# Kernel tuning notes

Measured on AMD Instinct MI355X. Metric: run time of the kernel, lower is better.

## Reference

```python
import jax, jax.numpy as jnp
import numpy as np

DIM = 1024
N_HEADS = 16
HEAD_DIM = DIM // N_HEADS


def setup_inputs() -> dict:
    key = jax.random.key(0)
    ks = jax.random.split(key, 5)
    B, L = 2, 2048
    q = jax.random.normal(ks[0], (B, L, DIM), dtype=jnp.float32)
    # nn.Linear weights: shape [out_features, in_features], applied as x @ W.T
    scale = 1.0 / np.sqrt(DIM)
    Wq = jax.random.normal(ks[1], (DIM, DIM), dtype=jnp.float32) * scale
    Wk = jax.random.normal(ks[2], (DIM, DIM), dtype=jnp.float32) * scale
    Wv = jax.random.normal(ks[3], (DIM, DIM), dtype=jnp.float32) * scale
    Wo = jax.random.normal(ks[4], (DIM, DIM), dtype=jnp.float32) * scale
    return {"q": q, "Wq": Wq, "Wk": Wk, "Wv": Wv, "Wo": Wo}


def reference(q, Wq, Wk, Wv, Wo):
    B, L, _ = q.shape
    kv = q  # self-attention (kv=None path)
    # projections: x @ W.T, then split heads: b l (h d) -> b h l d
    def split_heads(x):
        return x.reshape(B, L, N_HEADS, HEAD_DIM).transpose(0, 2, 1, 3)
    qh = split_heads(q @ Wq.T)
    kh = split_heads(kv @ Wk.T)
    vh = split_heads(kv @ Wv.T)
    # scaled dot-product attention; scale = sqrt(head_dim)
    scores = jnp.einsum('bhid,bhjd->bhij', qh, kh) / jnp.sqrt(
        jnp.asarray(HEAD_DIM, dtype=qh.dtype))
    attn = jax.nn.softmax(scores, axis=-1)
    out = jnp.einsum('bhij,bhjd->bhid', attn, vh)
    # b h l d -> b l (h d)
    out = out.transpose(0, 2, 1, 3).reshape(B, L, DIM)
    return out @ Wo.T
```

## Files before the change

### kernel.cpp

```cpp
#include <hip/hip_runtime.h>


#define DIMN 1024
#define NH 16
#define HD 64
#define BB 2
#define LL 2048

typedef float f32x4 __attribute__((ext_vector_type(4)));
typedef short s16x8 __attribute__((ext_vector_type(8)));

#define QSCALE 0.18033688011112042f

static __device__ __forceinline__ unsigned short f2bf(float f) {
  unsigned u = __float_as_uint(f);
  u += 0x7fffu + ((u >> 16) & 1u);
  return (unsigned short)(u >> 16);
}
static __device__ __forceinline__ unsigned packbf2(float lo, float hi) {
  return (unsigned)f2bf(lo) | ((unsigned)f2bf(hi) << 16);
}
static __device__ __forceinline__ float xexp2(float x) {
#if __has_builtin(__builtin_amdgcn_exp2f)
  return __builtin_amdgcn_exp2f(x);
#else
  return exp2f(x);
#endif
}
static __device__ __forceinline__ s16x8 cvt8(float4 a, float4 b) {
  s16x8 r;
  r[0] = (short)f2bf(a.x); r[1] = (short)f2bf(a.y);
  r[2] = (short)f2bf(a.z); r[3] = (short)f2bf(a.w);
  r[4] = (short)f2bf(b.x); r[5] = (short)f2bf(b.y);
  r[6] = (short)f2bf(b.z); r[7] = (short)f2bf(b.w);
  return r;
}
static __device__ __forceinline__ void gld16(const unsigned short* g,
                                             unsigned short* l) {
#if __has_builtin(__builtin_amdgcn_global_load_lds)
  __builtin_amdgcn_global_load_lds(
      (const __attribute__((address_space(1))) void*)g,
      (__attribute__((address_space(3))) void*)l, 16, 0, 0);
#else
  ((uint4*)l)[threadIdx.x & 63] = ((const uint4*)g)[0];
#endif
}

static __device__ __forceinline__ int vpos(int s128) {
  return (s128 & 0x60) | ((s128 & 0x0C) << 1) | ((s128 & 0x10) >> 2) | (s128 & 3);
}

__global__ __launch_bounds__(256) void cvt_all(
    const float* __restrict__ X, const float* __restrict__ Wq,
    const float* __restrict__ Wk, const float* __restrict__ Wv,
    const float* __restrict__ Wo, unsigned short* __restrict__ out) {
  const int blk = blockIdx.x;
  const float* src;
  unsigned short* dst;
  size_t off;
  if (blk < 2048) {
    src = X; dst = out; off = (size_t)blk * 2048;
  } else {
    int s = (blk - 2048) >> 9;
    src = (s == 0) ? Wq : (s == 1) ? Wk : (s == 2) ? Wv : Wo;
    dst = out + ((size_t)1 << 22) + (size_t)s * (1u << 20);
    off = (size_t)((blk - 2048) & 511) * 2048;
  }
  size_t i = off + (size_t)threadIdx.x * 8;
  float4 v0 = *(const float4*)(src + i);
  float4 v1 = *(const float4*)(src + i + 4);
  uint4 o;
  o.x = packbf2(v0.x, v0.y); o.y = packbf2(v0.z, v0.w);
  o.z = packbf2(v1.x, v1.y); o.w = packbf2(v1.z, v1.w);
  *(uint4*)(dst + i) = o;
}

__global__ __launch_bounds__(256) void gemm_qkv(
    const unsigned short* __restrict__ Xb, const unsigned short* __restrict__ Wb,
    unsigned short* __restrict__ Qb, unsigned short* __restrict__ Kb,
    unsigned short* __restrict__ VT) {
  __shared__ __align__(16) unsigned short Al[128 * 64];
  __shared__ __align__(16) unsigned short Bl[128 * 64];
  const int lin = blockIdx.x;
  const int xcd = lin & 7, sblk = lin >> 3;
  const int m0 = ((xcd & 3) * 8 + (sblk & 7)) * 128;
  const int n0g = ((xcd >> 2) * 12 + (sblk >> 3)) * 128;
  const int sel = n0g >> 10;
  const int tid = threadIdx.x;
  const int w = tid >> 6, lane = tid & 63;
  const int c = lane & 15, quad = lane >> 4;
  const int wm = (w & 1) * 64, wn = (w >> 1) * 64;

  f32x4 zero = {0.f, 0.f, 0.f, 0.f};
  f32x4 acc[4][4];
#pragma unroll
  for (int i = 0; i < 4; ++i)
#pragma unroll
    for (int j = 0; j < 4; ++j) acc[i][j] = zero;

  const int l8 = lane >> 3, p8 = lane & 7;
  const unsigned short* gA = Xb + (size_t)(m0 + w * 8 + l8) * DIMN + ((p8 ^ l8) * 8);
  const unsigned short* gB = Wb + (size_t)(n0g + w * 8 + l8) * DIMN + ((p8 ^ l8) * 8);
  unsigned short* lA = Al + (w * 8) * 64;
  unsigned short* lB = Bl + (w * 8) * 64;
  const int c7 = c & 7;

  for (int k0 = 0; k0 < DIMN; k0 += 64) {
    __syncthreads();
#pragma unroll
    for (int r = 0; r < 4; ++r) {
      gld16(gA + k0 + (size_t)(r * 32) * DIMN, lA + r * 32 * 64);
      gld16(gB + k0 + (size_t)(r * 32) * DIMN, lB + r * 32 * 64);
    }
    __syncthreads();
#pragma unroll
    for (int f = 0; f < 2; ++f) {
      const int rd = ((f * 4 + quad) ^ c7) * 8;
      s16x8 a[4], b[4];
#pragma unroll
      for (int i = 0; i < 4; ++i)
        a[i] = *(const s16x8*)&Al[(wm + i * 16 + c) * 64 + rd];
#pragma unroll
      for (int j = 0; j < 4; ++j)
        b[j] = *(const s16x8*)&Bl[(wn + j * 16 + c) * 64 + rd];
      if (sel != 2) {
#pragma unroll
        for (int i = 0; i < 4; ++i)
#pragma unroll
          for (int j = 0; j < 4; ++j)
            acc[i][j] = __builtin_amdgcn_mfma_f32_16x16x32_bf16(b[j], a[i], acc[i][j], 0, 0, 0);
      } else {
#pragma unroll
        for (int i = 0; i < 4; ++i)
#pragma unroll
          for (int j = 0; j < 4; ++j)
            acc[i][j] = __builtin_amdgcn_mfma_f32_16x16x32_bf16(a[i], b[j], acc[i][j], 0, 0, 0);
      }
    }
  }

  const int n0 = n0g & 1023;
  if (sel != 2) {
    unsigned short* Out = (sel == 0) ? Qb : Kb;
    const float scale = (sel == 0) ? QSCALE : 1.0f;
    const int bi = (m0 + wm) >> 11;
#pragma unroll
    for (int i = 0; i < 4; ++i) {
      const int li = (m0 + wm + i * 16 + c) & 2047;
#pragma unroll
      for (int j = 0; j < 4; ++j) {
        const int nq = n0 + wn + j * 16 + quad * 4;
        const int h = nq >> 6, d = nq & 63;
        uint2 st;
        st.x = packbf2(acc[i][j][0] * scale, acc[i][j][1] * scale);
        st.y = packbf2(acc[i][j][2] * scale, acc[i][j][3] * scale);
        *(uint2*)&Out[(((size_t)bi * NH + h) * LL + li) * HD + d] = st;
      }
    }
  } else {
    const int bi = m0 >> 11;
    const int mlo = m0 & 2047;
#pragma unroll
    for (int i = 0; i < 4; ++i) {
      const int pos = mlo + vpos(wm + i * 16 + quad * 4);
#pragma unroll
      for (int j = 0; j < 4; ++j) {
        const int nv = n0 + wn + j * 16 + c;
        const int h = nv >> 6, d = nv & 63;
        uint2 st;
        st.x = packbf2(acc[i][j][0], acc[i][j][1]);
        st.y = packbf2(acc[i][j][2], acc[i][j][3]);
        *(uint2*)&VT[(((size_t)bi * NH + h) * HD + d) * LL + pos] = st;
      }
    }
  }
}

__global__ __launch_bounds__(256) void gemm_o(
    const unsigned short* __restrict__ A, const unsigned short* __restrict__ Wob,
    float* __restrict__ Out) {
  __shared__ __align__(16) unsigned short Al[128 * 64];
  __shared__ __align__(16) unsigned short Bl[64 * 64];
  const int lin = blockIdx.x;
  const int xcd = lin & 7, sblk = lin >> 3;
  const int m0 = ((sblk >> 4) * 8 + xcd) * 128;
  const int n0 = (sblk & 15) * 64;
  const int tid = threadIdx.x;
  const int w = tid >> 6, lane = tid & 63;
  const int c = lane & 15, quad = lane >> 4;
  const int wm = (w & 1) * 64, wn = (w >> 1) * 32;

  f32x4 zero = {0.f, 0.f, 0.f, 0.f};
  f32x4 acc[4][2];
#pragma unroll
  for (int i = 0; i < 4; ++i)
#pragma unroll
    for (int j = 0; j < 2; ++j) acc[i][j] = zero;

  const int l8 = lane >> 3, p8 = lane & 7;
  const unsigned short* gA = A + (size_t)(m0 + w * 8 + l8) * DIMN + ((p8 ^ l8) * 8);
  const unsigned short* gB = Wob + (size_t)(n0 + w * 8 + l8) * DIMN + ((p8 ^ l8) * 8);
  unsigned short* lA = Al + (w * 8) * 64;
  unsigned short* lB = Bl + (w * 8) * 64;
  const int c7 = c & 7;

  for (int k0 = 0; k0 < DIMN; k0 += 64) {
    __syncthreads();
#pragma unroll
    for (int r = 0; r < 4; ++r)
      gld16(gA + k0 + (size_t)(r * 32) * DIMN, lA + r * 32 * 64);
#pragma unroll
    for (int r = 0; r < 2; ++r)
      gld16(gB + k0 + (size_t)(r * 32) * DIMN, lB + r * 32 * 64);
    __syncthreads();
#pragma unroll
    for (int f = 0; f < 2; ++f) {
      const int rd = ((f * 4 + quad) ^ c7) * 8;
      s16x8 a[4], b[2];
#pragma unroll
      for (int i = 0; i < 4; ++i)
        a[i] = *(const s16x8*)&Al[(wm + i * 16 + c) * 64 + rd];
#pragma unroll
      for (int j = 0; j < 2; ++j)
        b[j] = *(const s16x8*)&Bl[(wn + j * 16 + c) * 64 + rd];
#pragma unroll
      for (int i = 0; i < 4; ++i)
#pragma unroll
        for (int j = 0; j < 2; ++j)
          acc[i][j] = __builtin_amdgcn_mfma_f32_16x16x32_bf16(a[i], b[j], acc[i][j], 0, 0, 0);
    }
  }

#pragma unroll
  for (int i = 0; i < 4; ++i)
#pragma unroll
    for (int j = 0; j < 2; ++j)
#pragma unroll
      for (int r = 0; r < 4; ++r)
        Out[(size_t)(m0 + wm + i * 16 + quad * 4 + r) * DIMN + n0 + wn + j * 16 + c] =
            acc[i][j][r];
}

__global__ __launch_bounds__(512) void attn6(
    const unsigned short* __restrict__ Qb, const unsigned short* __restrict__ Kb,
    const unsigned short* __restrict__ VT, unsigned short* __restrict__ AO) {
  __shared__ __align__(16) unsigned short Kl[2 * 128 * 64];
  __shared__ __align__(16) unsigned short Vtl[2 * 64 * 128];

  const int lin = blockIdx.x;
  const int xcd = lin & 7, sblk = lin >> 3;
  const int bh = (sblk >> 4) * 8 + xcd;
  const int qi = sblk & 15;
  const int tid = threadIdx.x;
  const int w = tid >> 6, lane = tid & 63;
  const int c = lane & 15, quad = lane >> 4;
  const int q0 = qi * 128 + w * 16;

  const unsigned short* Qh = Qb + (size_t)bh * LL * HD;
  const unsigned short* Kh = Kb + (size_t)bh * LL * HD;
  const unsigned short* Vh = VT + (size_t)bh * HD * LL;

  s16x8 qf0 = *(const s16x8*)(Qh + (size_t)(q0 + c) * HD + quad * 8);
  s16x8 qf1 = *(const s16x8*)(Qh + (size_t)(q0 + c) * HD + 32 + quad * 8);

  f32x4 zero = {0.f, 0.f, 0.f, 0.f};
  f32x4 o[4];
  float lsum = 0.f;
#pragma unroll
  for (int dc = 0; dc < 4; ++dc) o[dc] = zero;

  const int l8 = lane >> 3, p8 = lane & 7;
  const unsigned short* gK = Kh + (size_t)(w * 16 + l8) * HD + ((p8 ^ l8) * 8);
  const int l16 = lane >> 4, p16 = lane & 15;
  const int vr0 = w * 8 + l16;
  const int vr1 = w * 8 + 4 + l16;
  const unsigned short* gV0 = Vh + (size_t)vr0 * LL + ((p16 ^ (vr0 & 15)) * 8);
  const unsigned short* gV1 = Vh + (size_t)vr1 * LL + ((p16 ^ (vr1 & 15)) * 8);

  const int kpa = (quad ^ (c & 7)) * 8;
  const int kpb = ((quad + 4) ^ (c & 7)) * 8;

#define STAGE(buf, k0)                                                        \
  do {                                                                        \
    unsigned short* lK_ = Kl + (buf) * (128 * 64) + (w * 16) * 64;            \
    unsigned short* lV_ = Vtl + (buf) * (64 * 128) + (w * 8) * 128;           \
    gld16(gK + (size_t)(k0) * HD, lK_);                                       \
    gld16(gK + (size_t)((k0) + 8) * HD, lK_ + 8 * 64);                        \
    gld16(gV0 + (k0), lV_);                                                   \
    gld16(gV1 + (k0), lV_ + 4 * 128);                                         \
  } while (0)

  STAGE(0, 0);

  for (int it = 0; it < LL / 128; ++it) {
    __syncthreads();
    if (it + 1 < LL / 128) STAGE((it + 1) & 1, (it + 1) * 128);
    const unsigned short* Kt = Kl + (it & 1) * (128 * 64);
    const unsigned short* Vt = Vtl + (it & 1) * (64 * 128);

#pragma unroll
    for (int g = 0; g < 2; ++g) {
      f32x4 s[4];
#pragma unroll
      for (int t4 = 0; t4 < 4; ++t4) {
        const unsigned short* kr = Kt + ((g * 4 + t4) * 16 + c) * 64;
        s16x8 kfa = *(const s16x8*)(kr + kpa);
        s16x8 kfb = *(const s16x8*)(kr + kpb);
        s[t4] = __builtin_amdgcn_mfma_f32_16x16x32_bf16(kfa, qf0, zero, 0, 0, 0);
        s[t4] = __builtin_amdgcn_mfma_f32_16x16x32_bf16(kfb, qf1, s[t4], 0, 0, 0);
      }
      float p[4][4];
      float acc_l = 0.f;
#pragma unroll
      for (int t4 = 0; t4 < 4; ++t4)
#pragma unroll
        for (int r = 0; r < 4; ++r) {
          float e = xexp2(s[t4][r]);
          p[t4][r] = e;
          acc_l += e;
        }
      lsum += acc_l;
#pragma unroll
      for (int kh = 0; kh < 2; ++kh) {
        const int kk = g * 2 + kh;
        unsigned pu[4];
        pu[0] = __builtin_amdgcn_perm(__float_as_uint(p[2 * kh][1]),
                                      __float_as_uint(p[2 * kh][0]), 0x07060302u);
        pu[1] = __builtin_amdgcn_perm(__float_as_uint(p[2 * kh][3]),
                                      __float_as_uint(p[2 * kh][2]), 0x07060302u);
        pu[2] = __builtin_amdgcn_perm(__float_as_uint(p[2 * kh + 1][1]),
                                      __float_as_uint(p[2 * kh + 1][0]), 0x07060302u);
        pu[3] = __builtin_amdgcn_perm(__float_as_uint(p[2 * kh + 1][3]),
                                      __float_as_uint(p[2 * kh + 1][2]), 0x07060302u);
        s16x8 pf = *(const s16x8*)pu;
#pragma unroll
        for (int dc = 0; dc < 4; ++dc) {
          s16x8 vf = *(const s16x8*)(Vt + (dc * 16 + c) * 128 + (((kk * 4 + quad) ^ c) * 8));
          o[dc] = __builtin_amdgcn_mfma_f32_16x16x32_bf16(vf, pf, o[dc], 0, 0, 0);
        }
      }
    }
  }
#undef STAGE

  const int bi = bh >> 4, h = bh & 15;
  float l = lsum;
  l += __shfl_xor(l, 16);
  l += __shfl_xor(l, 32);
  float inv = 1.0f / l;
  unsigned short* dst = AO + ((size_t)bi * LL + q0 + c) * DIMN + h * HD + quad * 4;
#pragma unroll
  for (int dc = 0; dc < 4; ++dc) {
    uint2 st;
    st.x = packbf2(o[dc][0] * inv, o[dc][1] * inv);
    st.y = packbf2(o[dc][2] * inv, o[dc][3] * inv);
    *(uint2*)(dst + dc * 16) = st;
  }
}

__global__ __launch_bounds__(64) void qkv_proj_f(
    const float* __restrict__ X, const float* __restrict__ Wq,
    const float* __restrict__ Wk, const float* __restrict__ Wv,
    unsigned short* __restrict__ Qb, unsigned short* __restrict__ Kb,
    unsigned short* __restrict__ VT) {
  const int m0 = blockIdx.x * 64;
  const int n0g = blockIdx.y * 64;
  const int sel = n0g >> 10;
  const int n0 = n0g & 1023;
  const float* W = (sel == 0) ? Wq : (sel == 1) ? Wk : Wv;
  const int lane = threadIdx.x;
  const int c = lane & 15, quad = lane >> 4;

  f32x4 zero = {0.f, 0.f, 0.f, 0.f};
  f32x4 acc[4][4];
#pragma unroll
  for (int i = 0; i < 4; ++i)
#pragma unroll
    for (int j = 0; j < 4; ++j) acc[i][j] = zero;

  const float* ab = X + (size_t)(m0 + c) * DIMN + quad * 8;
  const float* bb = W + (size_t)(n0 + c) * DIMN + quad * 8;

  for (int k0 = 0; k0 < DIMN; k0 += 32) {
    s16x8 a[4], b[4];
#pragma unroll
    for (int i = 0; i < 4; ++i) {
      const float* pp = ab + i * 16 * DIMN + k0;
      a[i] = cvt8(*(const float4*)pp, *(const float4*)(pp + 4));
    }
#pragma unroll
    for (int j = 0; j < 4; ++j) {
      const float* pp = bb + j * 16 * DIMN + k0;
      b[j] = cvt8(*(const float4*)pp, *(const float4*)(pp + 4));
    }
    if (sel != 2) {
#pragma unroll
      for (int i = 0; i < 4; ++i)
#pragma unroll
        for (int j = 0; j < 4; ++j)
          acc[i][j] = __builtin_amdgcn_mfma_f32_16x16x32_bf16(a[i], b[j], acc[i][j], 0, 0, 0);
    } else {
#pragma unroll
      for (int i = 0; i < 4; ++i)
#pragma unroll
        for (int j = 0; j < 4; ++j)
          acc[i][j] = __builtin_amdgcn_mfma_f32_16x16x32_bf16(b[j], a[i], acc[i][j], 0, 0, 0);
    }
  }

  if (sel != 2) {
    unsigned short* Out = (sel == 0) ? Qb : Kb;
    const float scale = (sel == 0) ? QSCALE : 1.0f;
#pragma unroll
    for (int i = 0; i < 4; ++i)
#pragma unroll
      for (int j = 0; j < 4; ++j)
#pragma unroll
        for (int r = 0; r < 4; ++r) {
          int row = m0 + i * 16 + quad * 4 + r;
          int nl = n0 + j * 16 + c;
          int bi = row >> 11, li = row & 2047;
          int h = nl >> 6, d = nl & 63;
          Out[(((size_t)bi * NH + h) * LL + li) * HD + d] = f2bf(acc[i][j][r] * scale);
        }
  } else {
#pragma unroll
    for (int i = 0; i < 4; ++i) {
#pragma unroll
      for (int j = 0; j < 4; ++j)
#pragma unroll
        for (int r = 0; r < 4; ++r) {
          int n = n0 + j * 16 + quad * 4 + r;
          int s128 = (m0 & 64) + i * 16 + c;
          int m = (m0 & ~127) + vpos(s128);
          int h = n >> 6, d = n & 63;
          int bi = m0 >> 11;
          VT[(((size_t)bi * NH + h) * HD + d) * LL + (m & 2047)] = f2bf(acc[i][j][r]);
        }
    }
  }
}

__global__ __launch_bounds__(64) void o_proj_f(
    const unsigned short* __restrict__ A, const float* __restrict__ Wo,
    float* __restrict__ Out) {
  const int m0 = blockIdx.x * 64, n0 = blockIdx.y * 64;
  const int lane = threadIdx.x;
  const int c = lane & 15, quad = lane >> 4;

  f32x4 zero = {0.f, 0.f, 0.f, 0.f};
  f32x4 acc[4][4];
#pragma unroll
  for (int i = 0; i < 4; ++i)
#pragma unroll
    for (int j = 0; j < 4; ++j) acc[i][j] = zero;

  const unsigned short* ab = A + (size_t)(m0 + c) * DIMN + quad * 8;
  const float* bb = Wo + (size_t)(n0 + c) * DIMN + quad * 8;

  for (int k0 = 0; k0 < DIMN; k0 += 32) {
    s16x8 a[4], b[4];
#pragma unroll
    for (int i = 0; i < 4; ++i) a[i] = *(const s16x8*)(ab + i * 16 * DIMN + k0);
#pragma unroll
    for (int j = 0; j < 4; ++j) {
      const float* pp = bb + j * 16 * DIMN + k0;
      b[j] = cvt8(*(const float4*)pp, *(const float4*)(pp + 4));
    }
#pragma unroll
    for (int i = 0; i < 4; ++i)
#pragma unroll
      for (int j = 0; j < 4; ++j)
        acc[i][j] = __builtin_amdgcn_mfma_f32_16x16x32_bf16(a[i], b[j], acc[i][j], 0, 0, 0);
  }

#pragma unroll
  for (int i = 0; i < 4; ++i)
#pragma unroll
    for (int j = 0; j < 4; ++j)
#pragma unroll
      for (int r = 0; r < 4; ++r)
        Out[(size_t)(m0 + i * 16 + quad * 4 + r) * DIMN + n0 + j * 16 + c] = acc[i][j][r];
}

extern "C" void kernel_launch(void* const* d_in, const int* in_sizes, int n_in,
                              void* d_out, int out_size, void* d_ws, size_t ws_size,
                              hipStream_t stream) {
  const float* X = (const float*)d_in[0];
  const float* Wq = (const float*)d_in[1];
  const float* Wk = (const float*)d_in[2];
  const float* Wv = (const float*)d_in[3];
  const float* Wo = (const float*)d_in[4];
  float* Out = (float*)d_out;

  const size_t M1 = (size_t)1 << 20;
  unsigned short* ws16 = (unsigned short*)d_ws;

  if (ws_size >= (size_t)48 * 1024 * 1024) {
    unsigned short* Xb = ws16;
    unsigned short* Wb = ws16 + 4 * M1;
    unsigned short* Qb = ws16 + 8 * M1;
    unsigned short* Kb = ws16 + 12 * M1;
    unsigned short* VT = ws16 + 16 * M1;
    unsigned short* AO = ws16 + 20 * M1;
    cvt_all<<<4096, 256, 0, stream>>>(X, Wq, Wk, Wv, Wo, ws16);
    gemm_qkv<<<768, 256, 0, stream>>>(Xb, Wb, Qb, Kb, VT);
    attn6<<<512, 512, 0, stream>>>(Qb, Kb, VT, AO);
    gemm_o<<<512, 256, 0, stream>>>(AO, Wb + 3 * M1, Out);
  } else {
    unsigned short* Qb = ws16;
    unsigned short* Kb = ws16 + 4 * M1;
    unsigned short* VT = ws16 + 8 * M1;
    unsigned short* AO = ws16 + 12 * M1;
    qkv_proj_f<<<dim3(64, 48), 64, 0, stream>>>(X, Wq, Wk, Wv, Qb, Kb, VT);
    attn6<<<512, 512, 0, stream>>>(Qb, Kb, VT, AO);
    o_proj_f<<<dim3(64, 16), 64, 0, stream>>>(AO, Wo, Out);
  }
}
```

Before: 179.9 us.

## Process two query tiles per wave in attention to reuse K/V fragments

The attention kernel now runs 4 waves (256 threads) per block instead of 8. Each wave handles two 16-row query tiles (rows qa and qa+64), so every K and V fragment read from LDS feeds two MFMAs. Each wave also stages twice as much K/V data per iteration. This halves LDS reads per MFMA and lowers barrier pressure, at the cost of roughly double the accumulator and score registers per wave and fewer waves per block to hide latency.

Result: faster. 174.2 us (-3.1%).

```diff
diff --git a/kernel.cpp b/kernel.cpp
--- a/kernel.cpp
+++ b/kernel.cpp
@@ -241,7 +241,7 @@
             acc[i][j][r];
 }
 
-__global__ __launch_bounds__(512) void attn6(
+__global__ __launch_bounds__(256, 2) void attn7(
     const unsigned short* __restrict__ Qb, const unsigned short* __restrict__ Kb,
     const unsigned short* __restrict__ VT, unsigned short* __restrict__ AO) {
   __shared__ __align__(16) unsigned short Kl[2 * 128 * 64];
@@ -254,40 +254,51 @@
   const int tid = threadIdx.x;
   const int w = tid >> 6, lane = tid & 63;
   const int c = lane & 15, quad = lane >> 4;
-  const int q0 = qi * 128 + w * 16;
+  const int qa = qi * 128 + w * 16;
+  const int qbr = qa + 64;
 
   const unsigned short* Qh = Qb + (size_t)bh * LL * HD;
   const unsigned short* Kh = Kb + (size_t)bh * LL * HD;
   const unsigned short* Vh = VT + (size_t)bh * HD * LL;
 
-  s16x8 qf0 = *(const s16x8*)(Qh + (size_t)(q0 + c) * HD + quad * 8);
-  s16x8 qf1 = *(const s16x8*)(Qh + (size_t)(q0 + c) * HD + 32 + quad * 8);
+  s16x8 qA0 = *(const s16x8*)(Qh + (size_t)(qa + c) * HD + quad * 8);
+  s16x8 qA1 = *(const s16x8*)(Qh + (size_t)(qa + c) * HD + 32 + quad * 8);
+  s16x8 qB0 = *(const s16x8*)(Qh + (size_t)(qbr + c) * HD + quad * 8);
+  s16x8 qB1 = *(const s16x8*)(Qh + (size_t)(qbr + c) * HD + 32 + quad * 8);
 
   f32x4 zero = {0.f, 0.f, 0.f, 0.f};
-  f32x4 o[4];
-  float lsum = 0.f;
-#pragma unroll
-  for (int dc = 0; dc < 4; ++dc) o[dc] = zero;
+  f32x4 oA[4], oB[4];
+  float lsumA = 0.f, lsumB = 0.f;
+#pragma unroll
+  for (int dc = 0; dc < 4; ++dc) { oA[dc] = zero; oB[dc] = zero; }
 
   const int l8 = lane >> 3, p8 = lane & 7;
-  const unsigned short* gK = Kh + (size_t)(w * 16 + l8) * HD + ((p8 ^ l8) * 8);
+  const unsigned short* gK = Kh + (size_t)(w * 32 + l8) * HD + ((p8 ^ l8) * 8);
   const int l16 = lane >> 4, p16 = lane & 15;
-  const int vr0 = w * 8 + l16;
-  const int vr1 = w * 8 + 4 + l16;
+  const int vr0 = w * 16 + l16;
+  const int vr1 = w * 16 + 4 + l16;
+  const int vr2 = w * 16 + 8 + l16;
+  const int vr3 = w * 16 + 12 + l16;
   const unsigned short* gV0 = Vh + (size_t)vr0 * LL + ((p16 ^ (vr0 & 15)) * 8);
   const unsigned short* gV1 = Vh + (size_t)vr1 * LL + ((p16 ^ (vr1 & 15)) * 8);
+  const unsigned short* gV2 = Vh + (size_t)vr2 * LL + ((p16 ^ (vr2 & 15)) * 8);
+  const unsigned short* gV3 = Vh + (size_t)vr3 * LL + ((p16 ^ (vr3 & 15)) * 8);
 
   const int kpa = (quad ^ (c & 7)) * 8;
   const int kpb = ((quad + 4) ^ (c & 7)) * 8;
 
 #define STAGE(buf, k0)                                                        \
   do {                                                                        \
-    unsigned short* lK_ = Kl + (buf) * (128 * 64) + (w * 16) * 64;            \
-    unsigned short* lV_ = Vtl + (buf) * (64 * 128) + (w * 8) * 128;           \
+    unsigned short* lK_ = Kl + (buf) * (128 * 64) + (w * 32) * 64;            \
+    unsigned short* lV_ = Vtl + (buf) * (64 * 128) + (w * 16) * 128;          \
     gld16(gK + (size_t)(k0) * HD, lK_);                                       \
     gld16(gK + (size_t)((k0) + 8) * HD, lK_ + 8 * 64);                        \
+    gld16(gK + (size_t)((k0) + 16) * HD, lK_ + 16 * 64);                      \
+    gld16(gK + (size_t)((k0) + 24) * HD, lK_ + 24 * 64);                      \
     gld16(gV0 + (k0), lV_);                                                   \
     gld16(gV1 + (k0), lV_ + 4 * 128);                                         \
+    gld16(gV2 + (k0), lV_ + 8 * 128);                                         \
+    gld16(gV3 + (k0), lV_ + 12 * 128);                                        \
   } while (0)
 
   STAGE(0, 0);
@@ -300,43 +311,57 @@
 
 #pragma unroll
     for (int g = 0; g < 2; ++g) {
-      f32x4 s[4];
+      f32x4 sA[4], sB[4];
 #pragma unroll
       for (int t4 = 0; t4 < 4; ++t4) {
         const unsigned short* kr = Kt + ((g * 4 + t4) * 16 + c) * 64;
         s16x8 kfa = *(const s16x8*)(kr + kpa);
         s16x8 kfb = *(const s16x8*)(kr + kpb);
-        s[t4] = __builtin_amdgcn_mfma_f32_16x16x32_bf16(kfa, qf0, zero, 0, 0, 0);
-        s[t4] = __builtin_amdgcn_mfma_f32_16x16x32_bf16(kfb, qf1, s[t4], 0, 0, 0);
+        sA[t4] = __builtin_amdgcn_mfma_f32_16x16x32_bf16(kfa, qA0, zero, 0, 0, 0);
+        sA[t4] = __builtin_amdgcn_mfma_f32_16x16x32_bf16(kfb, qA1, sA[t4], 0, 0, 0);
+        sB[t4] = __builtin_amdgcn_mfma_f32_16x16x32_bf16(kfa, qB0, zero, 0, 0, 0);
+        sB[t4] = __builtin_amdgcn_mfma_f32_16x16x32_bf16(kfb, qB1, sB[t4], 0, 0, 0);
       }
-      float p[4][4];
-      float acc_l = 0.f;
+      float pA[4][4], pB[4][4];
+      float accA = 0.f, accB = 0.f;
 #pragma unroll
       for (int t4 = 0; t4 < 4; ++t4)
 #pragma unroll
         for (int r = 0; r < 4; ++r) {
-          float e = xexp2(s[t4][r]);
-          p[t4][r] = e;
-          acc_l += e;
+          float eA = xexp2(sA[t4][r]);
+          float eB = xexp2(sB[t4][r]);
+          pA[t4][r] = eA; accA += eA;
+          pB[t4][r] = eB; accB += eB;
         }
-      lsum += acc_l;
+      lsumA += accA;
+      lsumB += accB;
 #pragma unroll
       for (int kh = 0; kh < 2; ++kh) {
         const int kk = g * 2 + kh;
-        unsigned pu[4];
-        pu[0] = __builtin_amdgcn_perm(__float_as_uint(p[2 * kh][1]),
-                                      __float_as_uint(p[2 * kh][0]), 0x07060302u);
-        pu[1] = __builtin_amdgcn_perm(__float_as_uint(p[2 * kh][3]),
-                                      __float_as_uint(p[2 * kh][2]), 0x07060302u);
-        pu[2] = __builtin_amdgcn_perm(__float_as_uint(p[2 * kh + 1][1]),
-                                      __float_as_uint(p[2 * kh + 1][0]), 0x07060302u);
-        pu[3] = __builtin_amdgcn_perm(__float_as_uint(p[2 * kh + 1][3]),
-                                      __float_as_uint(p[2 * kh + 1][2]), 0x07060302u);
-        s16x8 pf = *(const s16x8*)pu;
+        unsigned puA[4], puB[4];
+        puA[0] = __builtin_amdgcn_perm(__float_as_uint(pA[2 * kh][1]),
+                                       __float_as_uint(pA[2 * kh][0]), 0x07060302u);
+        puA[1] = __builtin_amdgcn_perm(__float_as_uint(pA[2 * kh][3]),
+                                       __float_as_uint(pA[2 * kh][2]), 0x07060302u);
+        puA[2] = __builtin_amdgcn_perm(__float_as_uint(pA[2 * kh + 1][1]),
+                                       __float_as_uint(pA[2 * kh + 1][0]), 0x07060302u);
+        puA[3] = __builtin_amdgcn_perm(__float_as_uint(pA[2 * kh + 1][3]),
+                                       __float_as_uint(pA[2 * kh + 1][2]), 0x07060302u);
+        puB[0] = __builtin_amdgcn_perm(__float_as_uint(pB[2 * kh][1]),
+                                       __float_as_uint(pB[2 * kh][0]), 0x07060302u);
+        puB[1] = __builtin_amdgcn_perm(__float_as_uint(pB[2 * kh][3]),
+                                       __float_as_uint(pB[2 * kh][2]), 0x07060302u);
+        puB[2] = __builtin_amdgcn_perm(__float_as_uint(pB[2 * kh + 1][1]),
+                                       __float_as_uint(pB[2 * kh + 1][0]), 0x07060302u);
+        puB[3] = __builtin_amdgcn_perm(__float_as_uint(pB[2 * kh + 1][3]),
+                                       __float_as_uint(pB[2 * kh + 1][2]), 0x07060302u);
+        s16x8 pfA = *(const s16x8*)puA;
+        s16x8 pfB = *(const s16x8*)puB;
 #pragma unroll
         for (int dc = 0; dc < 4; ++dc) {
           s16x8 vf = *(const s16x8*)(Vt + (dc * 16 + c) * 128 + (((kk * 4 + quad) ^ c) * 8));
-          o[dc] = __builtin_amdgcn_mfma_f32_16x16x32_bf16(vf, pf, o[dc], 0, 0, 0);
+          oA[dc] = __builtin_amdgcn_mfma_f32_16x16x32_bf16(vf, pfA, oA[dc], 0, 0, 0);
+          oB[dc] = __builtin_amdgcn_mfma_f32_16x16x32_bf16(vf, pfB, oB[dc], 0, 0, 0);
         }
       }
     }
@@ -344,17 +369,25 @@
 #undef STAGE
 
   const int bi = bh >> 4, h = bh & 15;
-  float l = lsum;
-  l += __shfl_xor(l, 16);
-  l += __shfl_xor(l, 32);
-  float inv = 1.0f / l;
-  unsigned short* dst = AO + ((size_t)bi * LL + q0 + c) * DIMN + h * HD + quad * 4;
+  float lA = lsumA;
+  lA += __shfl_xor(lA, 16);
+  lA += __shfl_xor(lA, 32);
+  float invA = 1.0f / lA;
+  float lB = lsumB;
+  lB += __shfl_xor(lB, 16);
+  lB += __shfl_xor(lB, 32);
+  float invB = 1.0f / lB;
+  unsigned short* dstA = AO + ((size_t)bi * LL + qa + c) * DIMN + h * HD + quad * 4;
+  unsigned short* dstB = AO + ((size_t)bi * LL + qbr + c) * DIMN + h * HD + quad * 4;
 #pragma unroll
   for (int dc = 0; dc < 4; ++dc) {
-    uint2 st;
-    st.x = packbf2(o[dc][0] * inv, o[dc][1] * inv);
-    st.y = packbf2(o[dc][2] * inv, o[dc][3] * inv);
-    *(uint2*)(dst + dc * 16) = st;
+    uint2 stA, stB;
+    stA.x = packbf2(oA[dc][0] * invA, oA[dc][1] * invA);
+    stA.y = packbf2(oA[dc][2] * invA, oA[dc][3] * invA);
+    stB.x = packbf2(oB[dc][0] * invB, oB[dc][1] * invB);
+    stB.y = packbf2(oB[dc][2] * invB, oB[dc][3] * invB);
+    *(uint2*)(dstA + dc * 16) = stA;
+    *(uint2*)(dstB + dc * 16) = stB;
   }
 }
 
@@ -505,7 +538,7 @@
     unsigned short* AO = ws16 + 20 * M1;
     cvt_all<<<4096, 256, 0, stream>>>(X, Wq, Wk, Wv, Wo, ws16);
     gemm_qkv<<<768, 256, 0, stream>>>(Xb, Wb, Qb, Kb, VT);
-    attn6<<<512, 512, 0, stream>>>(Qb, Kb, VT, AO);
+    attn7<<<512, 256, 0, stream>>>(Qb, Kb, VT, AO);
     gemm_o<<<512, 256, 0, stream>>>(AO, Wb + 3 * M1, Out);
   } else {
     unsigned short* Qb = ws16;
@@ -513,7 +546,7 @@
     unsigned short* VT = ws16 + 8 * M1;
     unsigned short* AO = ws16 + 12 * M1;
     qkv_proj_f<<<dim3(64, 48), 64, 0, stream>>>(X, Wq, Wk, Wv, Qb, Kb, VT);
-    attn6<<<512, 512, 0, stream>>>(Qb, Kb, VT, AO);
+    attn7<<<512, 256, 0, stream>>>(Qb, Kb, VT, AO);
     o_proj_f<<<dim3(64, 16), 64, 0, stream>>>(AO, Wo, Out);
   }
 }
```
